# Kernel optimization log

Measured on AMD Instinct MI355X. Metric: run time of the kernel, lower is better.

The kernel has to match this reference:

```python
import jax, jax.numpy as jnp
import numpy as np
import math

B, T, D, H = 2, 2048, 1024, 16


def _layernorm(x, gamma, beta, eps=1e-5):
    mu = jnp.mean(x, axis=-1, keepdims=True)
    var = jnp.var(x, axis=-1, keepdims=True)
    return (x - mu) * jax.lax.rsqrt(var + eps) * gamma + beta


def setup_inputs() -> dict:
    key = jax.random.key(0)
    ks = jax.random.split(key, 12)
    s = 1.0 / math.sqrt(D)
    return {
        "x": jax.random.normal(ks[0], (B, T, D), dtype=jnp.float32),
        "src_mask": jax.random.randint(ks[1], (B, T, T), 0, 2, dtype=jnp.int32),
        "ln_gamma": jnp.ones((D,), jnp.float32),
        "ln_beta": jnp.zeros((D,), jnp.float32),
        "Wq": jax.random.normal(ks[2], (D, D), jnp.float32) * s,
        "bq": jnp.zeros((D,), jnp.float32),
        "Wk": jax.random.normal(ks[3], (D, D), jnp.float32) * s,
        "bk": jnp.zeros((D,), jnp.float32),
        "Wv": jax.random.normal(ks[4], (D, D), jnp.float32) * s,
        "bv": jnp.zeros((D,), jnp.float32),
        "Wo": jax.random.normal(ks[5], (D, D), jnp.float32) * s,
        "bo": jnp.zeros((D,), jnp.float32),
    }


def reference(x, src_mask, ln_gamma, ln_beta, Wq, bq, Wk, bk, Wv, bv, Wo, bo):
    Bx, Tx, Dx = x.shape
    dh = Dx // H
    xn = _layernorm(x, ln_gamma, ln_beta)  # single LN; the three calls are identical
    q = (xn @ Wq + bq).reshape(Bx, Tx, H, dh)
    k = (xn @ Wk + bk).reshape(Bx, Tx, H, dh)
    v = (xn @ Wv + bv).reshape(Bx, Tx, H, dh)
    # scores: B, n, m, h
    attn = jnp.einsum('bnhd,bmhd->bnmh', q, k) / math.sqrt(dh)
    attn = attn + (1.0 - src_mask.astype(attn.dtype))[..., None] * -100000.0
    weight = jax.nn.softmax(attn, axis=2)
    y = jnp.einsum('bnmh,bmhd->bnhd', weight, v).reshape(Bx, Tx, Dx)
    return x + (y @ Wo + bo)
```

## Files before the change

### kernel.cpp

```cpp
#include <hip/hip_runtime.h>
#include <hip/hip_bf16.h>
#include <stdint.h>

#define Tq 2048
#define Dd 1024
#define Hh 16

typedef unsigned short u16;
typedef __attribute__((ext_vector_type(8))) short short8;
typedef __attribute__((ext_vector_type(4))) short s16x4;
typedef __attribute__((ext_vector_type(4))) float f32x4;

__device__ __forceinline__ u16 f2bf(float f) {
  union { float f; unsigned u; } v; v.f = f;
  unsigned r = (v.u + 0x7fffu + ((v.u >> 16) & 1u)) >> 16;
  return (u16)r;
}

__device__ __forceinline__ unsigned pk2bf(float a, float b) {
  __hip_bfloat162 h = __float22bfloat162_rn(float2{a, b});
  union { __hip_bfloat162 h; unsigned u; } c; c.h = h;
  return c.u;
}

__device__ __forceinline__ void load_lds16(const void* g, void* l) {
  __builtin_amdgcn_global_load_lds(
      (const __attribute__((address_space(1))) unsigned*)g,
      (__attribute__((address_space(3))) unsigned*)l, 16, 0, 0);
}

__device__ __forceinline__ f32x4 mfma_k32(short8 a, short8 b, f32x4 c) {
  return __builtin_amdgcn_mfma_f32_16x16x32_bf16(a, b, c, 0, 0, 0);
}
__device__ __forceinline__ f32x4 mfma_k16(s16x4 a, s16x4 b, f32x4 c) {
  return __builtin_amdgcn_mfma_f32_16x16x16bf16_1k(a, b, c, 0, 0, 0);
}

__global__ __launch_bounds__(256) void prep_kernel(
    const float* __restrict__ x, const float* __restrict__ gamma,
    const float* __restrict__ beta, u16* __restrict__ xn,
    const float* __restrict__ W0, const float* __restrict__ W1,
    const float* __restrict__ W2, const float* __restrict__ W3,
    u16* __restrict__ o_qkv, u16* __restrict__ o_o,
    const int* __restrict__ mask, uint32_t* __restrict__ bits,
    const float* __restrict__ bq, const float* __restrict__ bk,
    const float* __restrict__ bv, float* __restrict__ bias3) {
  __shared__ float t[32][33];
  int idx = blockIdx.x;
  int tid = threadIdx.x;
  if (idx < 4096) {
    int row = idx;
    const float4 v = ((const float4*)(x + (size_t)row * Dd))[tid];
    float s = v.x + v.y + v.z + v.w;
    float s2 = v.x * v.x + v.y * v.y + v.z * v.z + v.w * v.w;
#pragma unroll
    for (int off = 1; off < 64; off <<= 1) {
      s += __shfl_xor(s, off);
      s2 += __shfl_xor(s2, off);
    }
    int w = tid >> 6;
    if ((tid & 63) == 0) { t[0][w] = s; t[0][4 + w] = s2; }
    __syncthreads();
    s = t[0][0] + t[0][1] + t[0][2] + t[0][3];
    s2 = t[0][4] + t[0][5] + t[0][6] + t[0][7];
    float mu = s * (1.0f / Dd);
    float var = s2 * (1.0f / Dd) - mu * mu;
    float rstd = rsqrtf(var + 1e-5f);
    const float4 g = ((const float4*)gamma)[tid];
    const float4 bb = ((const float4*)beta)[tid];
    union { unsigned us[2]; uint2 u2; } o;
    o.us[0] = pk2bf((v.x - mu) * rstd * g.x + bb.x, (v.y - mu) * rstd * g.y + bb.y);
    o.us[1] = pk2bf((v.z - mu) * rstd * g.z + bb.z, (v.w - mu) * rstd * g.w + bb.w);
    *(uint2*)(xn + (size_t)row * Dd + tid * 4) = o.u2;
  } else if (idx < 8192) {
    int ti = idx - 4096;
    int z = ti >> 10, i = ti & 1023;
    const float* W = (z == 0) ? W0 : (z == 1) ? W1 : (z == 2) ? W2 : W3;
    u16* out = (z < 3) ? (o_qkv + (size_t)z * 1024 * 1024) : o_o;
    int k0 = (i & 31) * 32, n0 = (i >> 5) * 32;
    int tx = tid & 31, ty = tid >> 5;
#pragma unroll
    for (int j = 0; j < 4; ++j)
      t[ty + j * 8][tx] = W[(size_t)(k0 + ty + j * 8) * Dd + n0 + tx];
    __syncthreads();
#pragma unroll
    for (int j = 0; j < 4; ++j)
      out[(size_t)(n0 + ty + j * 8) * Dd + k0 + tx] = f2bf(t[tx][ty + j * 8]);
  } else if (idx < 9216) {
    int m = idx - 8192;
    int b = m >> 9, rest = m & 511;
    int qw = rest >> 3, kblk = rest & 7;
    int k = kblk * 256 + tid;
    const int* mp = mask + ((size_t)b * Tq + qw * 32) * Tq + k;
    uint32_t wv = 0;
#pragma unroll
    for (int j = 0; j < 32; ++j) wv |= (mp[(size_t)j * Tq] ? 1u : 0u) << j;
    bits[((size_t)b * 64 + qw) * Tq + k] = wv;
  } else {
    int i = (idx - 9216) * 256 + tid;
    float v = (i < 1024) ? bq[i] : (i < 2048) ? bk[i - 1024] : bv[i - 2048];
    bias3[i] = v;
  }
}

template <int MODE, int MT>
__global__ __launch_bounds__(256) void gemm_bt(
    const u16* __restrict__ A, const u16* __restrict__ Bt,
    const float* __restrict__ bias, const float* __restrict__ resid,
    void* __restrict__ Cout, u16* __restrict__ vtout, int ldc, int K) {
  constexpr int MTI = MT / 32;
  __shared__ u16 As[MT * 64];
  __shared__ u16 Bs[128 * 64];
  int tid = threadIdx.x;
  int lane = tid & 63, w = tid >> 6;
  int l16 = lane & 15, quad = lane >> 4;
  int x7 = l16 & 7;
  int wm = w >> 1, wn = w & 1;
  int m0 = blockIdx.y * MT, n0 = blockIdx.x * 128;
  int r8 = lane >> 3;
  int phys = lane & 7;
  int chunk = phys ^ r8;
  const u16* ga0 = A + (size_t)(m0 + r8) * K + chunk * 8;
  const u16* gb0 = Bt + (size_t)(n0 + r8) * K + chunk * 8;
  f32x4 acc[MTI][4];
#pragma unroll
  for (int i = 0; i < MTI; ++i)
#pragma unroll
    for (int j = 0; j < 4; ++j) acc[i][j] = {0.f, 0.f, 0.f, 0.f};

  for (int k0 = 0; k0 < K; k0 += 64) {
    __syncthreads();
#pragma unroll
    for (int c = 0; c < MT / 32; ++c) {
      int rb = c * 32 + w * 8;
      load_lds16(ga0 + (size_t)rb * K + k0, (char*)As + rb * 128);
    }
#pragma unroll
    for (int c = 0; c < 4; ++c) {
      int rb = c * 32 + w * 8;
      load_lds16(gb0 + (size_t)rb * K + k0, (char*)Bs + rb * 128);
    }
    __syncthreads();
    short8 af[MTI][2], bf[4][2];
#pragma unroll
    for (int mt = 0; mt < MTI; ++mt) {
      int row = wm * (MT / 2) + mt * 16 + l16;
#pragma unroll
      for (int ks = 0; ks < 2; ++ks)
        af[mt][ks] = *(const short8*)&As[row * 64 + (((ks << 2) | quad) ^ x7) * 8];
    }
#pragma unroll
    for (int nt = 0; nt < 4; ++nt) {
      int row = wn * 64 + nt * 16 + l16;
#pragma unroll
      for (int ks = 0; ks < 2; ++ks)
        bf[nt][ks] = *(const short8*)&Bs[row * 64 + (((ks << 2) | quad) ^ x7) * 8];
    }
#pragma unroll
    for (int ks = 0; ks < 2; ++ks)
#pragma unroll
      for (int mt = 0; mt < MTI; ++mt)
#pragma unroll
        for (int nt = 0; nt < 4; ++nt)
          acc[mt][nt] = mfma_k32(af[mt][ks], bf[nt][ks], acc[mt][nt]);
  }
#pragma unroll
  for (int nt = 0; nt < 4; ++nt) {
    int col = n0 + wn * 64 + nt * 16 + l16;
    float bv = bias[col];
    float scl = (MODE == 0 && col < 1024) ? 0.18033688011112042f : 1.0f;
#pragma unroll
    for (int mt = 0; mt < MTI; ++mt) {
      if (MODE == 0 && col >= 2048) {
        int d9 = col - 2048;
        int h = d9 >> 6, d = d9 & 63;
        int t0 = m0 + wm * (MT / 2) + mt * 16 + quad * 4;
        int b = t0 >> 11, tt = t0 & 2047;
        union { unsigned us[2]; uint2 u2; } o;
        o.us[0] = pk2bf(acc[mt][nt][0] + bv, acc[mt][nt][1] + bv);
        o.us[1] = pk2bf(acc[mt][nt][2] + bv, acc[mt][nt][3] + bv);
        *(uint2*)&vtout[((size_t)(b * Hh + h) * 64 + d) * Tq + tt] = o.u2;
      } else {
#pragma unroll
        for (int r = 0; r < 4; ++r) {
          int row = m0 + wm * (MT / 2) + mt * 16 + quad * 4 + r;
          size_t idx = (size_t)row * ldc + col;
          float vv = (acc[mt][nt][r] + bv) * scl;
          if (MODE == 0)
            ((u16*)Cout)[idx] = f2bf(vv);
          else
            ((float*)Cout)[idx] = vv + resid[idx];
        }
      }
    }
  }
}

__global__ __launch_bounds__(256, 4) void attn_kernel(
    const u16* __restrict__ qkv, const u16* __restrict__ vt,
    const uint32_t* __restrict__ mbits, u16* __restrict__ ybuf) {
  __shared__ u16 Ks[2][64 * 64];
  __shared__ u16 Vs[2][64 * 64];
  int tid = threadIdx.x;
  int lane = tid & 63, w = tid >> 6;
  int l16 = lane & 15, quad = lane >> 4;
  int x7 = l16 & 7;
  int qt = blockIdx.x, h = blockIdx.y, b = blockIdx.z;
  int qbase = qt * 64 + w * 16;
  const u16* Qb = qkv + (size_t)b * Tq * 3072 + h * 64;
  const u16* Kb = Qb + 1024;
  const u16* Vb = vt + ((size_t)(b * Hh + h)) * 64 * Tq;
  const uint32_t* Mrow = mbits + ((size_t)b * 64 + (qbase >> 5)) * Tq;
  int shift = (w & 1) * 16 + l16;

  int half = (w & 1) * 32;
  int r8 = lane >> 3;
  int phys = lane & 7;
  int chunk = phys ^ r8;
  bool isK = (w < 2);

  short8 qf[2];
#pragma unroll
  for (int ks = 0; ks < 2; ++ks)
    qf[ks] = *(const short8*)&Qb[(size_t)(qbase + l16) * 3072 + ks * 32 + quad * 8];

  f32x4 acc[4];
#pragma unroll
  for (int j = 0; j < 4; ++j) acc[j] = {0.f, 0.f, 0.f, 0.f};
  float lst = 0.f;

  auto stage = [&](int buf, int k0) {
    if (isK) {
#pragma unroll
      for (int j = 0; j < 4; ++j)
        load_lds16(Kb + (size_t)(k0 + half + j * 8 + r8) * 3072 + chunk * 8,
                   (char*)&Ks[buf][0] + (half + j * 8) * 128);
    } else {
#pragma unroll
      for (int j = 0; j < 4; ++j)
        load_lds16(Vb + (size_t)(half + j * 8 + r8) * Tq + k0 + chunk * 8,
                   (char*)&Vs[buf][0] + (half + j * 8) * 128);
    }
  };

  stage(0, 0);

  for (int kt = 0; kt < 32; ++kt) {
    int k0 = kt * 64;
    int buf = kt & 1;
    __syncthreads();
    uint32_t mv[4][4];
#pragma unroll
    for (int mt = 0; mt < 4; ++mt) {
      uint4 m4 = *(const uint4*)&Mrow[k0 + mt * 16 + quad * 4];
      mv[mt][0] = m4.x; mv[mt][1] = m4.y; mv[mt][2] = m4.z; mv[mt][3] = m4.w;
    }
    if (kt < 31) stage(buf ^ 1, k0 + 64);
    const u16* Kt = Ks[buf];
    const u16* Vtile = Vs[buf];
    f32x4 s[4];
#pragma unroll
    for (int i = 0; i < 4; ++i) s[i] = {0.f, 0.f, 0.f, 0.f};
#pragma unroll
    for (int mt = 0; mt < 4; ++mt)
#pragma unroll
      for (int ks = 0; ks < 2; ++ks) {
        short8 kf = *(const short8*)&Kt[(mt * 16 + l16) * 64 +
                                        (((ks << 2) | quad) ^ x7) * 8];
        s[mt] = mfma_k32(kf, qf[ks], s[mt]);
      }
    s16x4 pfrag[4];
#pragma unroll
    for (int mt = 0; mt < 4; ++mt) {
#pragma unroll
      for (int r = 0; r < 4; ++r) {
        float sv = ((mv[mt][r] >> shift) & 1u) ? s[mt][r] : -100000.0f;
        float p = exp2f(sv);
        s[mt][r] = p;
        lst += p;
      }
      union { unsigned us[2]; s16x4 v; } pk;
      pk.us[0] = pk2bf(s[mt][0], s[mt][1]);
      pk.us[1] = pk2bf(s[mt][2], s[mt][3]);
      pfrag[mt] = pk.v;
    }
#pragma unroll
    for (int mt = 0; mt < 4; ++mt) {
      int vch = ((2 * mt + (quad >> 1)) ^ x7) * 8 + (quad & 1) * 4;
#pragma unroll
      for (int nt2 = 0; nt2 < 4; ++nt2) {
        s16x4 vf = *(const s16x4*)&Vtile[(nt2 * 16 + l16) * 64 + vch];
        acc[nt2] = mfma_k16(pfrag[mt], vf, acc[nt2]);
      }
    }
  }
  lst += __shfl_xor(lst, 16);
  lst += __shfl_xor(lst, 32);
#pragma unroll
  for (int r = 0; r < 4; ++r) {
    float li = 1.0f / __shfl(lst, quad * 4 + r);
    size_t row = (size_t)b * Tq + qbase + quad * 4 + r;
#pragma unroll
    for (int nt2 = 0; nt2 < 4; ++nt2)
      ybuf[row * Dd + h * 64 + nt2 * 16 + l16] = f2bf(acc[nt2][r] * li);
  }
}

extern "C" void kernel_launch(void* const* d_in, const int* in_sizes, int n_in,
                              void* d_out, int out_size, void* d_ws, size_t ws_size,
                              hipStream_t stream) {
  (void)in_sizes; (void)n_in; (void)out_size; (void)ws_size;
  const float* x = (const float*)d_in[0];
  const int* mask = (const int*)d_in[1];
  const float* gamma = (const float*)d_in[2];
  const float* beta = (const float*)d_in[3];
  const float* Wq = (const float*)d_in[4];
  const float* bq = (const float*)d_in[5];
  const float* Wk = (const float*)d_in[6];
  const float* bk = (const float*)d_in[7];
  const float* Wv = (const float*)d_in[8];
  const float* bv = (const float*)d_in[9];
  const float* Wo = (const float*)d_in[10];
  const float* bo = (const float*)d_in[11];
  float* out = (float*)d_out;
  char* ws = (char*)d_ws;

  constexpr size_t SZ_XN = (size_t)4096 * 1024 * 2;
  constexpr size_t SZ_WTQ = (size_t)3072 * 1024 * 2;
  constexpr size_t SZ_WOT = (size_t)1024 * 1024 * 2;
  constexpr size_t SZ_B3 = 3072 * 4;
  constexpr size_t SZ_QKV = (size_t)4096 * 3072 * 2;
  constexpr size_t SZ_MBITS = (size_t)2 * 64 * 2048 * 4;
  constexpr size_t SZ_VT = (size_t)2 * 16 * 64 * 2048 * 2;
  size_t off = 0;
  u16* xn = (u16*)(ws + off); off += SZ_XN;
  u16* wtqkv = (u16*)(ws + off); off += SZ_WTQ;
  u16* wot = (u16*)(ws + off); off += SZ_WOT;
  float* bias3 = (float*)(ws + off); off += SZ_B3;
  u16* qkvb = (u16*)(ws + off); off += SZ_QKV;
  uint32_t* mbits = (uint32_t*)(ws + off); off += SZ_MBITS;
  u16* vtb = (u16*)(ws + off); off += SZ_VT;
  u16* ybuf = (u16*)(ws + off);

  prep_kernel<<<dim3(9228), dim3(256), 0, stream>>>(
      x, gamma, beta, xn, Wq, Wk, Wv, Wo, wtqkv, wot, mask, mbits, bq, bk, bv,
      bias3);
  gemm_bt<0, 128><<<dim3(24, 32), dim3(256), 0, stream>>>(
      xn, wtqkv, bias3, nullptr, qkvb, vtb, 3072, 1024);
  attn_kernel<<<dim3(32, 16, 2), dim3(256), 0, stream>>>(qkvb, vtb, mbits, ybuf);
  gemm_bt<1, 64><<<dim3(8, 64), dim3(256), 0, stream>>>(
      ybuf, wot, bo, x, out, nullptr, 1024, 1024);
}
```

Measured before the change: 258.6 us.

## Process 32 query rows per wave in attention to reuse K/V fragments

```diff
diff --git a/kernel.cpp b/kernel.cpp
--- a/kernel.cpp
+++ b/kernel.cpp
@@ -196,7 +196,7 @@
   }
 }
 
-__global__ __launch_bounds__(256, 4) void attn_kernel(
+__global__ __launch_bounds__(256, 2) void attn_kernel(
     const u16* __restrict__ qkv, const u16* __restrict__ vt,
     const uint32_t* __restrict__ mbits, u16* __restrict__ ybuf) {
   __shared__ u16 Ks[2][64 * 64];
@@ -206,12 +206,11 @@
   int l16 = lane & 15, quad = lane >> 4;
   int x7 = l16 & 7;
   int qt = blockIdx.x, h = blockIdx.y, b = blockIdx.z;
-  int qbase = qt * 64 + w * 16;
+  int qbase = qt * 128 + w * 32;
   const u16* Qb = qkv + (size_t)b * Tq * 3072 + h * 64;
   const u16* Kb = Qb + 1024;
   const u16* Vb = vt + ((size_t)(b * Hh + h)) * 64 * Tq;
   const uint32_t* Mrow = mbits + ((size_t)b * 64 + (qbase >> 5)) * Tq;
-  int shift = (w & 1) * 16 + l16;
 
   int half = (w & 1) * 32;
   int r8 = lane >> 3;
@@ -219,15 +218,20 @@
   int chunk = phys ^ r8;
   bool isK = (w < 2);
 
-  short8 qf[2];
-#pragma unroll
-  for (int ks = 0; ks < 2; ++ks)
-    qf[ks] = *(const short8*)&Qb[(size_t)(qbase + l16) * 3072 + ks * 32 + quad * 8];
-
-  f32x4 acc[4];
-#pragma unroll
-  for (int j = 0; j < 4; ++j) acc[j] = {0.f, 0.f, 0.f, 0.f};
-  float lst = 0.f;
+  short8 qf[2][2];
+#pragma unroll
+  for (int nt = 0; nt < 2; ++nt)
+#pragma unroll
+    for (int ks = 0; ks < 2; ++ks)
+      qf[nt][ks] = *(const short8*)&Qb[(size_t)(qbase + nt * 16 + l16) * 3072 +
+                                       ks * 32 + quad * 8];
+
+  f32x4 acc[2][4];
+#pragma unroll
+  for (int i = 0; i < 2; ++i)
+#pragma unroll
+    for (int j = 0; j < 4; ++j) acc[i][j] = {0.f, 0.f, 0.f, 0.f};
+  float lst[2] = {0.f, 0.f};
 
   auto stage = [&](int buf, int k0) {
     if (isK) {
@@ -258,31 +262,39 @@
     if (kt < 31) stage(buf ^ 1, k0 + 64);
     const u16* Kt = Ks[buf];
     const u16* Vtile = Vs[buf];
-    f32x4 s[4];
-#pragma unroll
-    for (int i = 0; i < 4; ++i) s[i] = {0.f, 0.f, 0.f, 0.f};
+    f32x4 s[4][2];
+#pragma unroll
+    for (int i = 0; i < 4; ++i)
+#pragma unroll
+      for (int j = 0; j < 2; ++j) s[i][j] = {0.f, 0.f, 0.f, 0.f};
 #pragma unroll
     for (int mt = 0; mt < 4; ++mt)
 #pragma unroll
       for (int ks = 0; ks < 2; ++ks) {
         short8 kf = *(const short8*)&Kt[(mt * 16 + l16) * 64 +
                                         (((ks << 2) | quad) ^ x7) * 8];
-        s[mt] = mfma_k32(kf, qf[ks], s[mt]);
+#pragma unroll
+        for (int nt = 0; nt < 2; ++nt)
+          s[mt][nt] = mfma_k32(kf, qf[nt][ks], s[mt][nt]);
       }
-    s16x4 pfrag[4];
-#pragma unroll
-    for (int mt = 0; mt < 4; ++mt) {
-#pragma unroll
-      for (int r = 0; r < 4; ++r) {
-        float sv = ((mv[mt][r] >> shift) & 1u) ? s[mt][r] : -100000.0f;
-        float p = exp2f(sv);
-        s[mt][r] = p;
-        lst += p;
+    s16x4 pfrag[4][2];
+#pragma unroll
+    for (int nt = 0; nt < 2; ++nt) {
+      int shift = nt * 16 + l16;
+#pragma unroll
+      for (int mt = 0; mt < 4; ++mt) {
+#pragma unroll
+        for (int r = 0; r < 4; ++r) {
+          float sv = ((mv[mt][r] >> shift) & 1u) ? s[mt][nt][r] : -100000.0f;
+          float p = exp2f(sv);
+          s[mt][nt][r] = p;
+          lst[nt] += p;
+        }
+        union { unsigned us[2]; s16x4 v; } pk;
+        pk.us[0] = pk2bf(s[mt][nt][0], s[mt][nt][1]);
+        pk.us[1] = pk2bf(s[mt][nt][2], s[mt][nt][3]);
+        pfrag[mt][nt] = pk.v;
       }
-      union { unsigned us[2]; s16x4 v; } pk;
-      pk.us[0] = pk2bf(s[mt][0], s[mt][1]);
-      pk.us[1] = pk2bf(s[mt][2], s[mt][3]);
-      pfrag[mt] = pk.v;
     }
 #pragma unroll
     for (int mt = 0; mt < 4; ++mt) {
@@ -290,20 +302,27 @@
 #pragma unroll
       for (int nt2 = 0; nt2 < 4; ++nt2) {
         s16x4 vf = *(const s16x4*)&Vtile[(nt2 * 16 + l16) * 64 + vch];
-        acc[nt2] = mfma_k16(pfrag[mt], vf, acc[nt2]);
+#pragma unroll
+        for (int nt = 0; nt < 2; ++nt)
+          acc[nt][nt2] = mfma_k16(pfrag[mt][nt], vf, acc[nt][nt2]);
       }
     }
   }
-  lst += __shfl_xor(lst, 16);
-  lst += __shfl_xor(lst, 32);
-#pragma unroll
-  for (int r = 0; r < 4; ++r) {
-    float li = 1.0f / __shfl(lst, quad * 4 + r);
-    size_t row = (size_t)b * Tq + qbase + quad * 4 + r;
-#pragma unroll
-    for (int nt2 = 0; nt2 < 4; ++nt2)
-      ybuf[row * Dd + h * 64 + nt2 * 16 + l16] = f2bf(acc[nt2][r] * li);
-  }
+#pragma unroll
+  for (int nt = 0; nt < 2; ++nt) {
+    lst[nt] += __shfl_xor(lst[nt], 16);
+    lst[nt] += __shfl_xor(lst[nt], 32);
+  }
+#pragma unroll
+  for (int nt = 0; nt < 2; ++nt)
+#pragma unroll
+    for (int r = 0; r < 4; ++r) {
+      float li = 1.0f / __shfl(lst[nt], quad * 4 + r);
+      size_t row = (size_t)b * Tq + qbase + nt * 16 + quad * 4 + r;
+#pragma unroll
+      for (int nt2 = 0; nt2 < 4; ++nt2)
+        ybuf[row * Dd + h * 64 + nt2 * 16 + l16] = f2bf(acc[nt][nt2][r] * li);
+    }
 }
 
 extern "C" void kernel_launch(void* const* d_in, const int* in_sizes, int n_in,
@@ -347,7 +366,7 @@
       bias3);
   gemm_bt<0, 128><<<dim3(24, 32), dim3(256), 0, stream>>>(
       xn, wtqkv, bias3, nullptr, qkvb, vtb, 3072, 1024);
-  attn_kernel<<<dim3(32, 16, 2), dim3(256), 0, stream>>>(qkvb, vtb, mbits, ybuf);
+  attn_kernel<<<dim3(16, 16, 2), dim3(256), 0, stream>>>(qkvb, vtb, mbits, ybuf);
   gemm_bt<1, 64><<<dim3(8, 64), dim3(256), 0, stream>>>(
       ybuf, wot, bo, x, out, nullptr, 1024, 1024);
 }
```

Result: no change. 254.1 us (-1.7%).
